# Optimization experiments

Measured on AMD Instinct MI355X. Metric: run time of the kernel, lower is better.

The kernel has to match this reference:

```python
import jax, jax.numpy as jnp
import numpy as np

B, C, S, NUM_D = 1, 1152, 64, 30  # activ is [B, C, S, S, S]; 30 disease heads


def setup_inputs() -> dict:
    key = jax.random.key(0)
    ks = jax.random.split(key, 5)
    activ = jax.random.normal(ks[0], (B, C, S, S, S), dtype=jnp.float32)
    score_w = jax.random.normal(ks[1], (NUM_D, C), dtype=jnp.float32) * (1.0 / np.sqrt(C))
    score_b = jax.random.normal(ks[2], (NUM_D,), dtype=jnp.float32) * 0.01
    head_w = jax.random.normal(ks[3], (NUM_D, C), dtype=jnp.float32) * 0.01
    head_b = jnp.zeros((NUM_D,), dtype=jnp.float32)
    # inv_sigmoid_temp(0.7): tau = 0.2 + 1.8*sigmoid(t) = 0.7 -> t = logit(0.5/1.8)
    t0 = float(np.log((0.5 / 1.8) / (1.0 - 0.5 / 1.8)))
    temp_logit = jnp.full((NUM_D,), t0, dtype=jnp.float32) + jax.random.normal(ks[4], (NUM_D,), dtype=jnp.float32) * 0.1
    return {"activ": activ, "score_w": score_w, "score_b": score_b,
            "head_w": head_w, "head_b": head_b, "temp_logit": temp_logit}


def reference(activ, score_w, score_b, head_w, head_b, temp_logit):
    b, c, d, h, w = activ.shape
    n = d * h * w
    feat = activ.reshape(b, c, n)                     # [B, C, N]
    # per-disease temperature: tau = 0.2 + 1.8*sigmoid(temp_logit)
    tau = 0.2 + 1.8 * jax.nn.sigmoid(temp_logit)      # [Dz]
    # batched 1x1x1 conv scorers across all 30 diseases at once
    logits = jnp.einsum('bcn,dc->bdn', feat, score_w) + score_b[None, :, None]
    logits = logits / tau[None, :, None]              # [B, Dz, N]
    # mask is all-ones (full volume) -> plain stable softmax with exp-arg clamp
    lmax = jnp.max(logits, axis=-1, keepdims=True)
    ew = jnp.exp(jnp.clip(logits - lmax, -60.0, 0.0))
    weights = ew / jnp.maximum(jnp.sum(ew, axis=-1, keepdims=True), 1e-12)
    # softmax-weighted pooling of the feature map per disease
    pooled = jnp.einsum('bcn,bdn->bdc', feat, weights)  # [B, Dz, C]
    pooled = jnp.where(jnp.isnan(pooled), jnp.zeros_like(pooled), pooled)
    # per-disease linear heads -> one logit per disease
    out = jnp.einsum('bdc,dc->bd', pooled, head_w) + head_b[None, :]
    out = jnp.where(jnp.isnan(out), jnp.zeros_like(out), out)
    return out  # [B, num_diseases]
```

## Files before the change

### kernel.cpp

```cpp
#include <hip/hip_runtime.h>

#define CDIM 1152
#define NDIS 30
#define NVOX (64*64*64)
#define NT   128
#define NBLK2 (NVOX/NT)
#define KSTEPS (CDIM/32)

#define AF_FLOATS 73728
#define PM_OFF AF_FLOATS
#define PD_OFF (PM_OFF + NDIS*NBLK2)
#define PN_OFF (PD_OFF + NDIS*NBLK2)

typedef float f32x4 __attribute__((ext_vector_type(4)));
typedef short bf16x8 __attribute__((ext_vector_type(8)));

__device__ inline short f2bf(float f) {
    unsigned u = __float_as_uint(f);
    unsigned r = (u + 0x7FFFu + ((u >> 16) & 1u)) >> 16;
    return (short)r;
}
__device__ inline float bf2f(short h) {
    return __uint_as_float(((unsigned)(unsigned short)h) << 16);
}
__device__ inline float inv_tau(float t) {
    float sig = 1.f / (1.f + expf(-t));
    return 1.f / (0.2f + 1.8f * sig);
}

__global__ void k_prep(const float* __restrict__ score_w,
                       const float* __restrict__ head_w,
                       short* __restrict__ afrag) {
    int idx = blockIdx.x * 256 + threadIdx.x;
    int e  = idx & 7;
    int l  = (idx >> 3) & 63;
    int p  = (idx >> 9) & 1;
    int mt = (idx >> 10) & 3;
    int t  = idx >> 12;
    if (t >= KSTEPS) return;
    int m = mt * 16 + (l & 15);
    int k = t * 32 + 8 * (l >> 4) + e;
    float w = 0.f;
    if (m < NDIS)          w = score_w[m * CDIM + k];
    else if (m < 2 * NDIS) w = head_w[(m - NDIS) * CDIM + k];
    short hi = f2bf(w);
    afrag[idx] = p ? f2bf(w - bf2f(hi)) : hi;
}

__global__ __launch_bounds__(256) void k_mfma(const float* __restrict__ activ,
                                              const short* __restrict__ afrag,
                                              const float* __restrict__ temp_logit,
                                              float* __restrict__ pm,
                                              float* __restrict__ pd,
                                              float* __restrict__ pn) {
    __shared__ float lds[2][32][NT];
    __shared__ float redm[32][8], rede[32][8], redh[32][8];

    const int tid  = threadIdx.x;
    const int lane = tid & 63;
    const int w    = tid >> 6;
    const int a    = lane >> 4;
    const int i16  = lane & 15;
    const int nb   = blockIdx.x * NT;

    f32x4 acc[4][2];
#pragma unroll
    for (int mt = 0; mt < 4; mt++)
#pragma unroll
        for (int nt = 0; nt < 2; nt++) acc[mt][nt] = (f32x4)0.f;

    auto stage = [&](int t, int b) {
        const int k0 = t * 32;
#pragma unroll
        for (int q = 0; q < 4; q++) {
            const int row = 8 * w + 2 * q;
            const float* g = activ + (size_t)(k0 + row + (lane >> 5)) * NVOX
                           + nb + (lane & 31) * 4;
            __builtin_amdgcn_global_load_lds(
                (const __attribute__((address_space(1))) unsigned int*)g,
                (__attribute__((address_space(3))) unsigned int*)&lds[b][row][0],
                16, 0, 0);
        }
    };

    stage(0, 0);
#pragma unroll 1
    for (int t = 0; t < KSTEPS; t++) {
        const int b = t & 1;
        __syncthreads();
        if (t + 1 < KSTEPS) stage(t + 1, 1 - b);

        bf16x8 ah[4], al[4];
#pragma unroll
        for (int mt = 0; mt < 4; mt++) {
            ah[mt] = ((const bf16x8*)afrag)[((t * 4 + mt) * 2 + 0) * 64 + lane];
            al[mt] = ((const bf16x8*)afrag)[((t * 4 + mt) * 2 + 1) * 64 + lane];
        }

        bf16x8 bh[2], bl[2];
#pragma unroll
        for (int nt = 0; nt < 2; nt++) {
            const int col = w * 32 + nt * 16 + i16;
#pragma unroll
            for (int e = 0; e < 8; e++) {
                float f = lds[b][8 * a + e][col];
                short hs = f2bf(f);
                float lf = f - bf2f(hs);
                bh[nt][e] = hs;
                bl[nt][e] = (short)(__float_as_uint(lf) >> 16);
            }
        }

#pragma unroll
        for (int mt = 0; mt < 4; mt++)
#pragma unroll
            for (int nt = 0; nt < 2; nt++) {
                acc[mt][nt] = __builtin_amdgcn_mfma_f32_16x16x32_bf16(ah[mt], bh[nt], acc[mt][nt], 0, 0, 0);
                acc[mt][nt] = __builtin_amdgcn_mfma_f32_16x16x32_bf16(ah[mt], bl[nt], acc[mt][nt], 0, 0, 0);
                acc[mt][nt] = __builtin_amdgcn_mfma_f32_16x16x32_bf16(al[mt], bh[nt], acc[mt][nt], 0, 0, 0);
            }
    }

    __syncthreads();
    float* ep = (float*)lds;
#pragma unroll
    for (int mt = 0; mt < 4; mt++)
#pragma unroll
        for (int nt = 0; nt < 2; nt++)
#pragma unroll
            for (int r = 0; r < 4; r++) {
                int m = mt * 16 + a * 4 + r;
                int n = w * 32 + nt * 16 + i16;
                ep[m * NT + n] = acc[mt][nt][r];
            }
    __syncthreads();

    const int d  = tid >> 3;
    const int j8 = tid & 7;
    if (d < NDIS) {
        float mx = -3.4e38f;
        for (int i = 0; i < 16; i++) mx = fmaxf(mx, ep[d * NT + j8 * 16 + i]);
        redm[d][j8] = mx;
    }
    __syncthreads();
    if (d < NDIS) {
        float mb = redm[d][0];
        for (int j = 1; j < 8; j++) mb = fmaxf(mb, redm[d][j]);
        float it = inv_tau(temp_logit[d]);
        float se = 0.f, sh = 0.f;
        for (int i = 0; i < 16; i++) {
            int ix = d * NT + j8 * 16 + i;
            float e = expf((ep[ix] - mb) * it);
            se += e;
            sh += e * ep[ix + NDIS * NT];
        }
        rede[d][j8] = se;
        redh[d][j8] = sh;
    }
    __syncthreads();
    if (tid < NDIS) {
        float mb = redm[tid][0];
        for (int j = 1; j < 8; j++) mb = fmaxf(mb, redm[tid][j]);
        float se = 0.f, sh = 0.f;
        for (int j = 0; j < 8; j++) { se += rede[tid][j]; sh += redh[tid][j]; }
        pm[tid * NBLK2 + blockIdx.x] = mb;
        pd[tid * NBLK2 + blockIdx.x] = se;
        pn[tid * NBLK2 + blockIdx.x] = sh;
    }
}

__global__ __launch_bounds__(256) void k_final(const float* __restrict__ pm,
                                               const float* __restrict__ pd,
                                               const float* __restrict__ pn,
                                               const float* __restrict__ temp_logit,
                                               const float* __restrict__ head_b,
                                               float* __restrict__ out) {
    const int d = blockIdx.x, tid = threadIdx.x;
    const int lane = tid & 63, wid = tid >> 6;
    __shared__ float sm[4], sd[4], sn[4];
    const float* bm = pm + d * NBLK2;
    const float* bd = pd + d * NBLK2;
    const float* bn = pn + d * NBLK2;

    float m[8], e[8], h[8];
#pragma unroll
    for (int i = 0; i < 8; i++) {
        int ix = tid + i * 256;
        m[i] = bm[ix]; e[i] = bd[ix]; h[i] = bn[ix];
    }
    float mx = m[0];
#pragma unroll
    for (int i = 1; i < 8; i++) mx = fmaxf(mx, m[i]);
#pragma unroll
    for (int off = 32; off > 0; off >>= 1) mx = fmaxf(mx, __shfl_xor(mx, off));
    if (lane == 0) sm[wid] = mx;
    __syncthreads();
    float M = fmaxf(fmaxf(sm[0], sm[1]), fmaxf(sm[2], sm[3]));

    float it = inv_tau(temp_logit[d]);
    float den = 0.f, num = 0.f;
#pragma unroll
    for (int i = 0; i < 8; i++) {
        float sc = expf((m[i] - M) * it);
        den += e[i] * sc;
        num += h[i] * sc;
    }
#pragma unroll
    for (int off = 32; off > 0; off >>= 1) {
        den += __shfl_xor(den, off);
        num += __shfl_xor(num, off);
    }
    if (lane == 0) { sd[wid] = den; sn[wid] = num; }
    __syncthreads();
    if (tid == 0) {
        float D = (sd[0] + sd[1]) + (sd[2] + sd[3]);
        float N = (sn[0] + sn[1]) + (sn[2] + sn[3]);
        float o = N / fmaxf(D, 1e-12f) + head_b[d];
        if (o != o) o = 0.f;
        out[d] = o;
    }
}

extern "C" void kernel_launch(void* const* d_in, const int* in_sizes, int n_in,
                              void* d_out, int out_size, void* d_ws, size_t ws_size,
                              hipStream_t stream) {
    const float* activ      = (const float*)d_in[0];
    const float* score_w    = (const float*)d_in[1];
    const float* head_w     = (const float*)d_in[3];
    const float* head_b     = (const float*)d_in[4];
    const float* temp_logit = (const float*)d_in[5];
    float* ws  = (float*)d_ws;
    float* out = (float*)d_out;

    short* afrag = (short*)ws;
    k_prep <<<576,   256, 0, stream>>>(score_w, head_w, afrag);
    k_mfma <<<NBLK2, 256, 0, stream>>>(activ, afrag, temp_logit,
                                       ws + PM_OFF, ws + PD_OFF, ws + PN_OFF);
    k_final<<<NDIS,  256, 0, stream>>>(ws + PM_OFF, ws + PD_OFF, ws + PN_OFF,
                                       temp_logit, head_b, out);
}
```

Before: 273.1 us.

## Load activation fragments directly into registers with register double-buffering

Replaces the LDS staging of activation tiles (global_load_lds plus a per-step __syncthreads) with direct per-lane global loads into registers. Two register buffers are ping-ponged, and the loop is unrolled by two so the next step's loads are issued before the current step's MFMAs. This removes the block-wide barrier and the LDS round trip from the main loop. In exchange each lane does strided scalar global loads (16 columns per row, spread across 8 rows), which may coalesce less well than the 16-byte LDS-direct loads and adds register pressure.

After: 302.5 us. 1.11x slower.

```diff
diff --git a/kernel.cpp b/kernel.cpp
--- a/kernel.cpp
+++ b/kernel.cpp
@@ -47,13 +47,49 @@
     afrag[idx] = p ? f2bf(w - bf2f(hi)) : hi;
 }
 
+#define LOADB(TT, BD)                                                          \
+    {                                                                          \
+        const float* bp = bstep + (size_t)(TT) * (32 * (size_t)NVOX);          \
+        _Pragma("unroll") for (int e = 0; e < 8; e++) {                        \
+            BD[e]     = bp[(size_t)e * NVOX];                                  \
+            BD[8 + e] = bp[(size_t)e * NVOX + 16];                             \
+        }                                                                      \
+    }
+
+#define BODY(T, BC, BN)                                                        \
+    {                                                                          \
+        bf16x8 ah[4], al[4];                                                   \
+        _Pragma("unroll") for (int mt = 0; mt < 4; mt++) {                     \
+            ah[mt] = afp[(size_t)((T) * 8 + mt * 2 + 0) * 64 + lane];          \
+            al[mt] = afp[(size_t)((T) * 8 + mt * 2 + 1) * 64 + lane];          \
+        }                                                                      \
+        __builtin_amdgcn_sched_barrier(0);                                     \
+        int tn = ((T) + 1 < KSTEPS) ? (T) + 1 : KSTEPS - 1;                    \
+        LOADB(tn, BN);                                                         \
+        bf16x8 bh[2], bl[2];                                                   \
+        _Pragma("unroll") for (int nt = 0; nt < 2; nt++)                       \
+            _Pragma("unroll") for (int e = 0; e < 8; e++) {                    \
+                float f = BC[nt * 8 + e];                                      \
+                short hs = f2bf(f);                                            \
+                bh[nt][e] = hs;                                                \
+                float lf = f - bf2f(hs);                                       \
+                bl[nt][e] = (short)(__float_as_uint(lf) >> 16);                \
+            }                                                                  \
+        _Pragma("unroll") for (int mt = 0; mt < 4; mt++)                       \
+            _Pragma("unroll") for (int nt = 0; nt < 2; nt++) {                 \
+                acc[mt][nt] = __builtin_amdgcn_mfma_f32_16x16x32_bf16(ah[mt], bh[nt], acc[mt][nt], 0, 0, 0); \
+                acc[mt][nt] = __builtin_amdgcn_mfma_f32_16x16x32_bf16(ah[mt], bl[nt], acc[mt][nt], 0, 0, 0); \
+                acc[mt][nt] = __builtin_amdgcn_mfma_f32_16x16x32_bf16(al[mt], bh[nt], acc[mt][nt], 0, 0, 0); \
+            }                                                                  \
+    }
+
 __global__ __launch_bounds__(256) void k_mfma(const float* __restrict__ activ,
                                               const short* __restrict__ afrag,
                                               const float* __restrict__ temp_logit,
                                               float* __restrict__ pm,
                                               float* __restrict__ pd,
                                               float* __restrict__ pn) {
-    __shared__ float lds[2][32][NT];
+    __shared__ float ep[64][NT];
     __shared__ float redm[32][8], rede[32][8], redh[32][8];
 
     const int tid  = threadIdx.x;
@@ -63,66 +99,24 @@
     const int i16  = lane & 15;
     const int nb   = blockIdx.x * NT;
 
+    const bf16x8* afp = (const bf16x8*)afrag;
+    const float* bstep = activ + (size_t)(8 * a) * NVOX + nb + w * 32 + i16;
+
     f32x4 acc[4][2];
 #pragma unroll
     for (int mt = 0; mt < 4; mt++)
 #pragma unroll
         for (int nt = 0; nt < 2; nt++) acc[mt][nt] = (f32x4)0.f;
 
-    auto stage = [&](int t, int b) {
-        const int k0 = t * 32;
-#pragma unroll
-        for (int q = 0; q < 4; q++) {
-            const int row = 8 * w + 2 * q;
-            const float* g = activ + (size_t)(k0 + row + (lane >> 5)) * NVOX
-                           + nb + (lane & 31) * 4;
-            __builtin_amdgcn_global_load_lds(
-                (const __attribute__((address_space(1))) unsigned int*)g,
-                (__attribute__((address_space(3))) unsigned int*)&lds[b][row][0],
-                16, 0, 0);
-        }
-    };
-
-    stage(0, 0);
+    float B0[16], B1[16];
+    LOADB(0, B0);
+
 #pragma unroll 1
-    for (int t = 0; t < KSTEPS; t++) {
-        const int b = t & 1;
-        __syncthreads();
-        if (t + 1 < KSTEPS) stage(t + 1, 1 - b);
-
-        bf16x8 ah[4], al[4];
-#pragma unroll
-        for (int mt = 0; mt < 4; mt++) {
-            ah[mt] = ((const bf16x8*)afrag)[((t * 4 + mt) * 2 + 0) * 64 + lane];
-            al[mt] = ((const bf16x8*)afrag)[((t * 4 + mt) * 2 + 1) * 64 + lane];
-        }
-
-        bf16x8 bh[2], bl[2];
-#pragma unroll
-        for (int nt = 0; nt < 2; nt++) {
-            const int col = w * 32 + nt * 16 + i16;
-#pragma unroll
-            for (int e = 0; e < 8; e++) {
-                float f = lds[b][8 * a + e][col];
-                short hs = f2bf(f);
-                float lf = f - bf2f(hs);
-                bh[nt][e] = hs;
-                bl[nt][e] = (short)(__float_as_uint(lf) >> 16);
-            }
-        }
-
-#pragma unroll
-        for (int mt = 0; mt < 4; mt++)
-#pragma unroll
-            for (int nt = 0; nt < 2; nt++) {
-                acc[mt][nt] = __builtin_amdgcn_mfma_f32_16x16x32_bf16(ah[mt], bh[nt], acc[mt][nt], 0, 0, 0);
-                acc[mt][nt] = __builtin_amdgcn_mfma_f32_16x16x32_bf16(ah[mt], bl[nt], acc[mt][nt], 0, 0, 0);
-                acc[mt][nt] = __builtin_amdgcn_mfma_f32_16x16x32_bf16(al[mt], bh[nt], acc[mt][nt], 0, 0, 0);
-            }
-    }
-
-    __syncthreads();
-    float* ep = (float*)lds;
+    for (int t = 0; t < KSTEPS; t += 2) {
+        BODY(t,     B0, B1);
+        BODY(t + 1, B1, B0);
+    }
+
 #pragma unroll
     for (int mt = 0; mt < 4; mt++)
 #pragma unroll
@@ -131,7 +125,7 @@
             for (int r = 0; r < 4; r++) {
                 int m = mt * 16 + a * 4 + r;
                 int n = w * 32 + nt * 16 + i16;
-                ep[m * NT + n] = acc[mt][nt][r];
+                ep[m][n] = acc[mt][nt][r];
             }
     __syncthreads();
 
@@ -139,7 +133,7 @@
     const int j8 = tid & 7;
     if (d < NDIS) {
         float mx = -3.4e38f;
-        for (int i = 0; i < 16; i++) mx = fmaxf(mx, ep[d * NT + j8 * 16 + i]);
+        for (int i = 0; i < 16; i++) mx = fmaxf(mx, ep[d][j8 * 16 + i]);
         redm[d][j8] = mx;
     }
     __syncthreads();
@@ -149,10 +143,9 @@
         float it = inv_tau(temp_logit[d]);
         float se = 0.f, sh = 0.f;
         for (int i = 0; i < 16; i++) {
-            int ix = d * NT + j8 * 16 + i;
-            float e = expf((ep[ix] - mb) * it);
+            float e = expf((ep[d][j8 * 16 + i] - mb) * it);
             se += e;
-            sh += e * ep[ix + NDIS * NT];
+            sh += e * ep[d + NDIS][j8 * 16 + i];
         }
         rede[d][j8] = se;
         redh[d][j8] = sh;
```
